# Performance work log

Hardware: AMD Instinct MI355X
Metric: run time of the kernel (lower is better)

## Reference

```python
import jax, jax.numpy as jnp
import numpy as np

NUM_HEADS = 8
KEY_SIZE = 64
VALUE_SIZE = 64
NUM_GROUPS = 3 * NUM_HEADS  # 24
C = NUM_HEADS * (2 * KEY_SIZE + VALUE_SIZE)  # 1536
EPS = 1e-5


def setup_inputs() -> dict:
    key = jax.random.key(0)
    k1, k2, k3 = jax.random.split(key, 3)
    x = jax.random.normal(k1, (8, C, 32, 32), dtype=jnp.float32)
    # GroupNorm affine params (torch default ones/zeros, perturbed for non-trivial grads)
    gn_weight = 1.0 + 0.1 * jax.random.normal(k2, (C,), dtype=jnp.float32)
    gn_bias = 0.1 * jax.random.normal(k3, (C,), dtype=jnp.float32)
    return {"x": x, "gn_weight": gn_weight, "gn_bias": gn_bias}


def _group_norm(x, weight, bias):
    B, Cc, H, W = x.shape
    xg = x.reshape(B, NUM_GROUPS, -1)  # [B, G, (C/G)*H*W]
    mean = jnp.mean(xg, axis=-1, keepdims=True)
    var = jnp.var(xg, axis=-1, keepdims=True)
    xn = ((xg - mean) * jax.lax.rsqrt(var + EPS)).reshape(B, Cc, H, W)
    return xn * weight[:, None, None] + bias[:, None, None]


def reference(x, gn_weight, gn_bias):
    NH, KS, VS = NUM_HEADS, KEY_SIZE, VALUE_SIZE
    B, Cc, H, W = x.shape
    xn = _group_norm(x, gn_weight, gn_bias)
    xr = xn.reshape(B, NH, 2 * KS + VS, H * W)  # [B, NH, 2KS+VS, NK]
    k = xr[:, :, :KS]            # [B, NH, KS, NK]
    q = xr[:, :, KS:2 * KS]      # [B, NH, KS, NK]
    v = xr[:, :, 2 * KS:]        # [B, NH, VS, NK]
    # saliency = q^T @ k / sqrt(KS) -> [B, NH, NKq, NKk]
    sal = jnp.einsum('bhcq,bhck->bhqk', q, k) / jnp.sqrt(jnp.float32(KS))
    mask = jax.nn.softmax(sal, axis=-1)
    # out = v @ mask^T -> [B, NH, VS, NKq]
    out = jnp.einsum('bhvk,bhqk->bhvq', v, mask)
    return out.reshape(B, NH * VS, H, W)
```

## Files before the change

### kernel.cpp

```cpp
#include <hip/hip_runtime.h>
#include <hip/hip_bf16.h>


typedef __attribute__((ext_vector_type(8))) short bf16x8;
typedef __attribute__((ext_vector_type(4))) float f32x4;
typedef __attribute__((ext_vector_type(16))) float f32x16;
typedef unsigned short u16;
typedef unsigned int u32;

#define SM_SCALE 0.18033688f
#define SM_OFF   8.0f

__device__ __forceinline__ u32 pack2(float a, float b) {
    union { float f; u32 u; } ua, ub; ua.f = a; ub.f = b;
    return __builtin_amdgcn_perm(ub.u + 0x8000u, ua.u + 0x8000u, 0x07060302u);
}
union BB { uint4 u; bf16x8 v; };

__device__ __forceinline__ f32x16 zero16() {
    f32x16 z;
#pragma unroll
    for (int i = 0; i < 16; ++i) z[i] = 0.f;
    return z;
}

__device__ __forceinline__ void swap32(u32 a, u32 b, int hi, u32& ret0, u32& ret1) {
#if __has_builtin(__builtin_amdgcn_permlane32_swap)
    (void)hi;
    auto sw = __builtin_amdgcn_permlane32_swap(a, b, false, false);
    ret0 = sw[0]; ret1 = sw[1];
#else
    u32 pa = __shfl_xor(a, 32), pb = __shfl_xor(b, 32);
    ret0 = hi ? pb : a;
    ret1 = hi ? b : pa;
#endif
}

__global__ __launch_bounds__(256) void gn_partial(const float* __restrict__ x,
                                                  float* __restrict__ partials) {
    int blk = blockIdx.x;
    const float4* p = (const float4*)(x + (size_t)blk * 8192);
    int t = threadIdx.x;
    float s1a = 0.f, s2a = 0.f, s1b = 0.f, s2b = 0.f;
#pragma unroll
    for (int i = 0; i < 8; i += 2) {
        float4 va = p[t + i * 256];
        float4 vb = p[t + (i + 1) * 256];
        s1a += va.x + va.y + va.z + va.w;
        s2a += va.x*va.x + va.y*va.y + va.z*va.z + va.w*va.w;
        s1b += vb.x + vb.y + vb.z + vb.w;
        s2b += vb.x*vb.x + vb.y*vb.y + vb.z*vb.z + vb.w*vb.w;
    }
    float s1 = s1a + s1b, s2 = s2a + s2b;
    for (int off = 32; off > 0; off >>= 1) {
        s1 += __shfl_down(s1, off);
        s2 += __shfl_down(s2, off);
    }
    __shared__ float a1[4], a2[4];
    int wave = t >> 6, lane = t & 63;
    if (lane == 0) { a1[wave] = s1; a2[wave] = s2; }
    __syncthreads();
    if (t == 0) {
        partials[blk * 2 + 0] = a1[0] + a1[1] + a1[2] + a1[3];
        partials[blk * 2 + 1] = a2[0] + a2[1] + a2[2] + a2[3];
    }
}

__device__ __forceinline__ void group_stats(const float* __restrict__ partials,
                                            int bg, float& mean, float& rstd) {
    float s1 = 0.f, s2 = 0.f;
#pragma unroll
    for (int j = 0; j < 8; ++j) {
        s1 += partials[(bg * 8 + j) * 2 + 0];
        s2 += partials[(bg * 8 + j) * 2 + 1];
    }
    mean = s1 * (1.f / 65536.f);
    float var = s2 * (1.f / 65536.f) - mean * mean;
    rstd = rsqrtf(var + 1e-5f);
}

__global__ __launch_bounds__(256) void pack_kernel(
    const float* __restrict__ x, const float* __restrict__ gamma,
    const float* __restrict__ beta, const float* __restrict__ partials,
    u16* __restrict__ Qn, u16* __restrict__ Kn, u16* __restrict__ Vn)
{
    const int st = blockIdx.x >> 6, pair = blockIdx.x & 63;
    const int b = pair >> 3, h = pair & 7;
    const float* xb = x + (size_t)b * 1536 * 1024;
    float ms[3], rs[3];
    group_stats(partials, b * 24 + 3 * h + 0, ms[0], rs[0]);
    group_stats(partials, b * 24 + 3 * h + 1, ms[1], rs[1]);
    group_stats(partials, b * 24 + 3 * h + 2, ms[2], rs[2]);

    const int t = threadIdx.x;
    __shared__ u32 Tsh[64][33];

    const int cp = t >> 4;
    const int s4 = (t & 15) * 4;
    const int sgl = st * 64 + s4;

    for (int t2 = 0; t2 < 2; ++t2) {
        if (t2) __syncthreads();
#pragma unroll
        for (int dc = 0; dc < 2; ++dc) {
            int cg0 = h * 192 + t2 * 64 + dc * 32 + cp * 2;
            float4 va = *(const float4*)(xb + (size_t)cg0 * 1024 + sgl);
            float4 vb = *(const float4*)(xb + (size_t)(cg0 + 1) * 1024 + sgl);
            float w0 = gamma[cg0] * rs[t2],     b0 = beta[cg0] - ms[t2] * w0;
            float w1 = gamma[cg0 + 1] * rs[t2], b1 = beta[cg0 + 1] - ms[t2] * w1;
            int col = dc * 16 + cp;
            Tsh[s4 + 0][col] = pack2(va.x * w0 + b0, vb.x * w1 + b1);
            Tsh[s4 + 1][col] = pack2(va.y * w0 + b0, vb.y * w1 + b1);
            Tsh[s4 + 2][col] = pack2(va.z * w0 + b0, vb.z * w1 + b1);
            Tsh[s4 + 3][col] = pack2(va.w * w0 + b0, vb.w * w1 + b1);
        }
        __syncthreads();
        u16* dst = (t2 ? Qn : Kn) + (size_t)pair * 65536 + (size_t)st * 64 * 64;
#pragma unroll
        for (int p = 0; p < 2; ++p) {
            int row = p * 32 + (t >> 3);
            int c8 = (t & 7) * 4;
            uint4 o;
            o.x = Tsh[row][c8 + 0]; o.y = Tsh[row][c8 + 1];
            o.z = Tsh[row][c8 + 2]; o.w = Tsh[row][c8 + 3];
            *(uint4*)(dst + (size_t)row * 64 + c8 * 2) = o;
        }
    }
    {
#pragma unroll
        for (int dc = 0; dc < 4; ++dc) {
            int c = dc * 16 + (t >> 4);
            int cg = h * 192 + 128 + c;
            float4 v = *(const float4*)(xb + (size_t)cg * 1024 + sgl);
            float wsc = gamma[cg] * rs[2];
            float bsc = beta[cg] - ms[2] * wsc;
            uint2 o;
            o.x = pack2(v.x * wsc + bsc, v.y * wsc + bsc);
            o.y = pack2(v.z * wsc + bsc, v.w * wsc + bsc);
            *(uint2*)(Vn + (size_t)pair * 65536 + (size_t)c * 1024 + sgl) = o;
        }
    }
}

__global__ __launch_bounds__(256, 2) void attn_kernel(
    const u16* __restrict__ Qn, const u16* __restrict__ Kn,
    const u16* __restrict__ Vn, float* __restrict__ out)
{
    const int bid = blockIdx.x;
    const int qt = bid >> 6;
    const int pair = bid & 63;
    const int tid = threadIdx.x;
    const int w = tid >> 6;
    const int lane = tid & 63;
    const int li = lane & 31;
    const int hi = lane >> 5;

    __shared__ uint4 KT[2][512];
    __shared__ uint4 VT[2][512];

    const u16* Qp = Qn + (size_t)pair * 65536;
    const u16* Kp = Kn + (size_t)pair * 65536;
    const u16* Vp = Vn + (size_t)pair * 65536;

    const int j0 = tid * 2;
    const int srow = j0 >> 3;
    const int sch  = j0 & 7;
    const int sx   = srow & 7;
    const int idx0 = srow * 8 + (sch ^ sx);
    const int idx1 = srow * 8 + ((sch + 1) ^ sx);

    const int q0 = qt * 128 + w * 32;
    bf16x8 bq[4];
#pragma unroll
    for (int cs = 0; cs < 4; ++cs)
        bq[cs] = *(const bf16x8*)(Qp + (size_t)(q0 + li) * 64 + cs * 16 + hi * 8);

    f32x16 oacc[2];
    oacc[0] = zero16(); oacc[1] = zero16();
    float lsum = 0.f;

    const int x7 = li & 7;

    uint4 s0, s1, s2, s3;
    s0 = *(const uint4*)(Kp + (size_t)j0 * 8);
    s1 = *(const uint4*)(Kp + (size_t)j0 * 8 + 8);
    s2 = *(const uint4*)(Vp + (size_t)srow * 1024 + sch * 8);
    s3 = *(const uint4*)(Vp + (size_t)srow * 1024 + sch * 8 + 8);
    KT[0][idx0] = s0; KT[0][idx1] = s1;
    VT[0][idx0] = s2; VT[0][idx1] = s3;
    __syncthreads();

#pragma unroll 2
    for (int kt = 0; kt < 16; ++kt) {
        const int cur = kt & 1;
        if (kt < 15) {
            s0 = *(const uint4*)(Kp + (size_t)(kt + 1) * 4096 + j0 * 8);
            s1 = *(const uint4*)(Kp + (size_t)(kt + 1) * 4096 + j0 * 8 + 8);
            s2 = *(const uint4*)(Vp + (size_t)srow * 1024 + (kt + 1) * 64 + sch * 8);
            s3 = *(const uint4*)(Vp + (size_t)srow * 1024 + (kt + 1) * 64 + sch * 8 + 8);
        }

        f32x16 sf[2];
#pragma unroll
        for (int kf = 0; kf < 2; ++kf) {
            bf16x8 ak[4];
#pragma unroll
            for (int cs = 0; cs < 4; ++cs)
                ak[cs] = ((const BB*)&KT[cur][(kf * 32 + li) * 8 + ((cs * 2 + hi) ^ x7)])->v;
            f32x16 acc = zero16();
            __builtin_amdgcn_s_setprio(1);
#pragma unroll
            for (int cs = 0; cs < 4; ++cs)
                acc = __builtin_amdgcn_mfma_f32_32x32x16_bf16(ak[cs], bq[cs], acc, 0, 0, 0);
            __builtin_amdgcn_s_setprio(0);
            sf[kf] = acc;
        }

        BB pbv[4];
#pragma unroll
        for (int kf = 0; kf < 2; ++kf)
#pragma unroll
            for (int s = 0; s < 2; ++s) {
                float p0 = exp2f(__builtin_fmaf(sf[kf][8 * s + 0], SM_SCALE, -SM_OFF));
                float p1 = exp2f(__builtin_fmaf(sf[kf][8 * s + 1], SM_SCALE, -SM_OFF));
                float p2 = exp2f(__builtin_fmaf(sf[kf][8 * s + 2], SM_SCALE, -SM_OFF));
                float p3 = exp2f(__builtin_fmaf(sf[kf][8 * s + 3], SM_SCALE, -SM_OFF));
                float p4 = exp2f(__builtin_fmaf(sf[kf][8 * s + 4], SM_SCALE, -SM_OFF));
                float p5 = exp2f(__builtin_fmaf(sf[kf][8 * s + 5], SM_SCALE, -SM_OFF));
                float p6 = exp2f(__builtin_fmaf(sf[kf][8 * s + 6], SM_SCALE, -SM_OFF));
                float p7 = exp2f(__builtin_fmaf(sf[kf][8 * s + 7], SM_SCALE, -SM_OFF));
                lsum += ((p0 + p1) + (p2 + p3)) + ((p4 + p5) + (p6 + p7));
                u32 Pa = pack2(p0, p1), Pb = pack2(p2, p3);
                u32 Pc = pack2(p4, p5), Pd = pack2(p6, p7);
                u32 w0, w1, w2, w3;
                swap32(Pa, Pc, hi, w0, w2);
                swap32(Pb, Pd, hi, w1, w3);
                pbv[kf * 2 + s].u = uint4{w0, w1, w2, w3};
            }

#pragma unroll
        for (int vf = 0; vf < 2; ++vf) {
            bf16x8 av[4];
#pragma unroll
            for (int ks = 0; ks < 4; ++ks)
                av[ks] = ((const BB*)&VT[cur][(vf * 32 + li) * 8 + ((ks * 2 + hi) ^ x7)])->v;
            __builtin_amdgcn_s_setprio(1);
#pragma unroll
            for (int ks = 0; ks < 4; ++ks)
                oacc[vf] = __builtin_amdgcn_mfma_f32_32x32x16_bf16(av[ks], pbv[ks].v, oacc[vf], 0, 0, 0);
            __builtin_amdgcn_s_setprio(0);
        }

        if (kt < 15) {
            const int nxt = cur ^ 1;
            KT[nxt][idx0] = s0; KT[nxt][idx1] = s1;
            VT[nxt][idx0] = s2; VT[nxt][idx1] = s3;
        }
        __syncthreads();
    }

    lsum += __shfl_xor(lsum, 32);
    float invl = 1.f / lsum;
    float* ob = out + (size_t)pair * 65536 + q0 + li;
#pragma unroll
    for (int vf = 0; vf < 2; ++vf)
#pragma unroll
        for (int r = 0; r < 16; ++r) {
            int v = vf * 32 + (r & 3) + 8 * (r >> 2) + 4 * hi;
            ob[(size_t)v * 1024] = oacc[vf][r] * invl;
        }
}

extern "C" void kernel_launch(void* const* d_in, const int* in_sizes, int n_in,
                              void* d_out, int out_size, void* d_ws, size_t ws_size,
                              hipStream_t stream) {
    const float* x     = (const float*)d_in[0];
    const float* gamma = (const float*)d_in[1];
    const float* beta  = (const float*)d_in[2];
    float* out = (float*)d_out;

    float* partials = (float*)d_ws;
    u16* Qn = (u16*)((char*)d_ws + 32768);
    u16* Kn = Qn + (size_t)64 * 65536;
    u16* Vn = Kn + (size_t)64 * 65536;

    gn_partial<<<1536, 256, 0, stream>>>(x, partials);
    pack_kernel<<<1024, 256, 0, stream>>>(x, gamma, beta, partials, Qn, Kn, Vn);
    attn_kernel<<<512, 256, 0, stream>>>(Qn, Kn, Vn, out);
}
```

Baseline: 131.6 us.

## Fuse GroupNorm normalize and bf16 pack into attention kernel, drop pack pass

```diff
diff --git a/kernel.cpp b/kernel.cpp
--- a/kernel.cpp
+++ b/kernel.cpp
@@ -79,101 +79,70 @@
     rstd = rsqrtf(var + 1e-5f);
 }
 
-__global__ __launch_bounds__(256) void pack_kernel(
+__global__ __launch_bounds__(256, 2) void attn_fused(
     const float* __restrict__ x, const float* __restrict__ gamma,
     const float* __restrict__ beta, const float* __restrict__ partials,
-    u16* __restrict__ Qn, u16* __restrict__ Kn, u16* __restrict__ Vn)
-{
-    const int st = blockIdx.x >> 6, pair = blockIdx.x & 63;
-    const int b = pair >> 3, h = pair & 7;
-    const float* xb = x + (size_t)b * 1536 * 1024;
-    float ms[3], rs[3];
-    group_stats(partials, b * 24 + 3 * h + 0, ms[0], rs[0]);
-    group_stats(partials, b * 24 + 3 * h + 1, ms[1], rs[1]);
-    group_stats(partials, b * 24 + 3 * h + 2, ms[2], rs[2]);
-
-    const int t = threadIdx.x;
-    __shared__ u32 Tsh[64][33];
-
-    const int cp = t >> 4;
-    const int s4 = (t & 15) * 4;
-    const int sgl = st * 64 + s4;
-
-    for (int t2 = 0; t2 < 2; ++t2) {
-        if (t2) __syncthreads();
-#pragma unroll
-        for (int dc = 0; dc < 2; ++dc) {
-            int cg0 = h * 192 + t2 * 64 + dc * 32 + cp * 2;
-            float4 va = *(const float4*)(xb + (size_t)cg0 * 1024 + sgl);
-            float4 vb = *(const float4*)(xb + (size_t)(cg0 + 1) * 1024 + sgl);
-            float w0 = gamma[cg0] * rs[t2],     b0 = beta[cg0] - ms[t2] * w0;
-            float w1 = gamma[cg0 + 1] * rs[t2], b1 = beta[cg0 + 1] - ms[t2] * w1;
-            int col = dc * 16 + cp;
-            Tsh[s4 + 0][col] = pack2(va.x * w0 + b0, vb.x * w1 + b1);
-            Tsh[s4 + 1][col] = pack2(va.y * w0 + b0, vb.y * w1 + b1);
-            Tsh[s4 + 2][col] = pack2(va.z * w0 + b0, vb.z * w1 + b1);
-            Tsh[s4 + 3][col] = pack2(va.w * w0 + b0, vb.w * w1 + b1);
-        }
-        __syncthreads();
-        u16* dst = (t2 ? Qn : Kn) + (size_t)pair * 65536 + (size_t)st * 64 * 64;
-#pragma unroll
-        for (int p = 0; p < 2; ++p) {
-            int row = p * 32 + (t >> 3);
-            int c8 = (t & 7) * 4;
-            uint4 o;
-            o.x = Tsh[row][c8 + 0]; o.y = Tsh[row][c8 + 1];
-            o.z = Tsh[row][c8 + 2]; o.w = Tsh[row][c8 + 3];
-            *(uint4*)(dst + (size_t)row * 64 + c8 * 2) = o;
-        }
-    }
-    {
-#pragma unroll
-        for (int dc = 0; dc < 4; ++dc) {
-            int c = dc * 16 + (t >> 4);
-            int cg = h * 192 + 128 + c;
-            float4 v = *(const float4*)(xb + (size_t)cg * 1024 + sgl);
-            float wsc = gamma[cg] * rs[2];
-            float bsc = beta[cg] - ms[2] * wsc;
-            uint2 o;
-            o.x = pack2(v.x * wsc + bsc, v.y * wsc + bsc);
-            o.y = pack2(v.z * wsc + bsc, v.w * wsc + bsc);
-            *(uint2*)(Vn + (size_t)pair * 65536 + (size_t)c * 1024 + sgl) = o;
-        }
-    }
-}
-
-__global__ __launch_bounds__(256, 2) void attn_kernel(
-    const u16* __restrict__ Qn, const u16* __restrict__ Kn,
-    const u16* __restrict__ Vn, float* __restrict__ out)
+    float* __restrict__ out)
 {
     const int bid = blockIdx.x;
     const int qt = bid >> 6;
     const int pair = bid & 63;
+    const int b = pair >> 3, h = pair & 7;
+    const float* xb = x + (size_t)b * 1536 * 1024;
     const int tid = threadIdx.x;
     const int w = tid >> 6;
     const int lane = tid & 63;
     const int li = lane & 31;
     const int hi = lane >> 5;
 
+    float ms[3], rs[3];
+    group_stats(partials, b * 24 + 3 * h + 0, ms[0], rs[0]);
+    group_stats(partials, b * 24 + 3 * h + 1, ms[1], rs[1]);
+    group_stats(partials, b * 24 + 3 * h + 2, ms[2], rs[2]);
+
     __shared__ uint4 KT[2][512];
     __shared__ uint4 VT[2][512];
 
-    const u16* Qp = Qn + (size_t)pair * 65536;
-    const u16* Kp = Kn + (size_t)pair * 65536;
-    const u16* Vp = Vn + (size_t)pair * 65536;
-
-    const int j0 = tid * 2;
-    const int srow = j0 >> 3;
-    const int sch  = j0 & 7;
-    const int sx   = srow & 7;
-    const int idx0 = srow * 8 + (sch ^ sx);
-    const int idx1 = srow * 8 + ((sch + 1) ^ sx);
+    const int sr = tid & 63;
+    const int cc0 = tid >> 6;
+    float kw[16], kb[16];
+#pragma unroll
+    for (int u = 0; u < 16; ++u) {
+        int c = ((u < 8) ? cc0 : (cc0 + 4)) * 8 + (u & 7);
+        int cg = h * 192 + c;
+        kw[u] = gamma[cg] * rs[0];
+        kb[u] = beta[cg] - ms[0] * kw[u];
+    }
+    const int vcg = h * 192 + 128 + sr;
+    const float vw = gamma[vcg] * rs[2];
+    const float vb = beta[vcg] - ms[2] * vw;
+
+    const int kx = sr & 7;
+    const int kidx0 = sr * 8 + (cc0 ^ kx);
+    const int kidx1 = sr * 8 + ((cc0 + 4) ^ kx);
+    const int vidx0 = sr * 8 + ((cc0 * 2) ^ kx);
+    const int vidx1 = sr * 8 + ((cc0 * 2 + 1) ^ kx);
+
+    const float* kbase = xb + (size_t)(h * 192) * 1024 + sr;
+    const float* vbase = xb + (size_t)vcg * 1024 + cc0 * 16;
 
     const int q0 = qt * 128 + w * 32;
     bf16x8 bq[4];
 #pragma unroll
-    for (int cs = 0; cs < 4; ++cs)
-        bq[cs] = *(const bf16x8*)(Qp + (size_t)(q0 + li) * 64 + cs * 16 + hi * 8);
+    for (int cs = 0; cs < 4; ++cs) {
+        u32 qq[4];
+#pragma unroll
+        for (int jp = 0; jp < 4; ++jp) {
+            int cg = h * 192 + 64 + cs * 16 + hi * 8 + jp * 2;
+            float w0 = gamma[cg] * rs[1],     b0 = beta[cg] - ms[1] * w0;
+            float w1 = gamma[cg + 1] * rs[1], b1 = beta[cg + 1] - ms[1] * w1;
+            float a0 = xb[(size_t)cg * 1024 + q0 + li];
+            float a1 = xb[(size_t)(cg + 1) * 1024 + q0 + li];
+            qq[jp] = pack2(__builtin_fmaf(a0, w0, b0), __builtin_fmaf(a1, w1, b1));
+        }
+        BB tb; tb.u = uint4{qq[0], qq[1], qq[2], qq[3]};
+        bq[cs] = tb.v;
+    }
 
     f32x16 oacc[2];
     oacc[0] = zero16(); oacc[1] = zero16();
@@ -181,24 +150,70 @@
 
     const int x7 = li & 7;
 
-    uint4 s0, s1, s2, s3;
-    s0 = *(const uint4*)(Kp + (size_t)j0 * 8);
-    s1 = *(const uint4*)(Kp + (size_t)j0 * 8 + 8);
-    s2 = *(const uint4*)(Vp + (size_t)srow * 1024 + sch * 8);
-    s3 = *(const uint4*)(Vp + (size_t)srow * 1024 + sch * 8 + 8);
-    KT[0][idx0] = s0; KT[0][idx1] = s1;
-    VT[0][idx0] = s2; VT[0][idx1] = s3;
+    float rk[16], rv[16];
+#define LOAD_TILE(KT_)                                                        \
+    {                                                                         \
+        const float* kp = kbase + (KT_) * 64;                                 \
+        _Pragma("unroll")                                                     \
+        for (int u = 0; u < 16; ++u) {                                        \
+            int c = ((u < 8) ? cc0 : (cc0 + 4)) * 8 + (u & 7);                \
+            rk[u] = kp[(size_t)c * 1024];                                     \
+        }                                                                     \
+        const float* vp = vbase + (KT_) * 64;                                 \
+        _Pragma("unroll")                                                     \
+        for (int f = 0; f < 4; ++f) {                                         \
+            float4 vq = *(const float4*)(vp + f * 4);                         \
+            rv[f * 4 + 0] = vq.x; rv[f * 4 + 1] = vq.y;                       \
+            rv[f * 4 + 2] = vq.z; rv[f * 4 + 3] = vq.w;                       \
+        }                                                                     \
+    }
+#define COMMIT_TILE(BUF_)                                                     \
+    {                                                                         \
+        uint4 ka, kc, va, vc;                                                 \
+        ka.x = pack2(__builtin_fmaf(rk[0], kw[0], kb[0]),                     \
+                     __builtin_fmaf(rk[1], kw[1], kb[1]));                    \
+        ka.y = pack2(__builtin_fmaf(rk[2], kw[2], kb[2]),                     \
+                     __builtin_fmaf(rk[3], kw[3], kb[3]));                    \
+        ka.z = pack2(__builtin_fmaf(rk[4], kw[4], kb[4]),                     \
+                     __builtin_fmaf(rk[5], kw[5], kb[5]));                    \
+        ka.w = pack2(__builtin_fmaf(rk[6], kw[6], kb[6]),                     \
+                     __builtin_fmaf(rk[7], kw[7], kb[7]));                    \
+        kc.x = pack2(__builtin_fmaf(rk[8], kw[8], kb[8]),                     \
+                     __builtin_fmaf(rk[9], kw[9], kb[9]));                    \
+        kc.y = pack2(__builtin_fmaf(rk[10], kw[10], kb[10]),                  \
+                     __builtin_fmaf(rk[11], kw[11], kb[11]));                 \
+        kc.z = pack2(__builtin_fmaf(rk[12], kw[12], kb[12]),                  \
+                     __builtin_fmaf(rk[13], kw[13], kb[13]));                 \
+        kc.w = pack2(__builtin_fmaf(rk[14], kw[14], kb[14]),                  \
+                     __builtin_fmaf(rk[15], kw[15], kb[15]));                 \
+        va.x = pack2(__builtin_fmaf(rv[0], vw, vb),                           \
+                     __builtin_fmaf(rv[1], vw, vb));                          \
+        va.y = pack2(__builtin_fmaf(rv[2], vw, vb),                           \
+                     __builtin_fmaf(rv[3], vw, vb));                          \
+        va.z = pack2(__builtin_fmaf(rv[4], vw, vb),                           \
+                     __builtin_fmaf(rv[5], vw, vb));                          \
+        va.w = pack2(__builtin_fmaf(rv[6], vw, vb),                           \
+                     __builtin_fmaf(rv[7], vw, vb));                          \
+        vc.x = pack2(__builtin_fmaf(rv[8], vw, vb),                           \
+                     __builtin_fmaf(rv[9], vw, vb));                          \
+        vc.y = pack2(__builtin_fmaf(rv[10], vw, vb),                          \
+                     __builtin_fmaf(rv[11], vw, vb));                         \
+        vc.z = pack2(__builtin_fmaf(rv[12], vw, vb),                          \
+                     __builtin_fmaf(rv[13], vw, vb));                         \
+        vc.w = pack2(__builtin_fmaf(rv[14], vw, vb),                          \
+                     __builtin_fmaf(rv[15], vw, vb));                         \
+        KT[BUF_][kidx0] = ka; KT[BUF_][kidx1] = kc;                           \
+        VT[BUF_][vidx0] = va; VT[BUF_][vidx1] = vc;                           \
+    }
+
+    LOAD_TILE(0);
+    COMMIT_TILE(0);
     __syncthreads();
 
 #pragma unroll 2
     for (int kt = 0; kt < 16; ++kt) {
         const int cur = kt & 1;
-        if (kt < 15) {
-            s0 = *(const uint4*)(Kp + (size_t)(kt + 1) * 4096 + j0 * 8);
-            s1 = *(const uint4*)(Kp + (size_t)(kt + 1) * 4096 + j0 * 8 + 8);
-            s2 = *(const uint4*)(Vp + (size_t)srow * 1024 + (kt + 1) * 64 + sch * 8);
-            s3 = *(const uint4*)(Vp + (size_t)srow * 1024 + (kt + 1) * 64 + sch * 8 + 8);
-        }
+        if (kt < 15) LOAD_TILE(kt + 1);
 
         f32x16 sf[2];
 #pragma unroll
@@ -251,11 +266,7 @@
             __builtin_amdgcn_s_setprio(0);
         }
 
-        if (kt < 15) {
-            const int nxt = cur ^ 1;
-            KT[nxt][idx0] = s0; KT[nxt][idx1] = s1;
-            VT[nxt][idx0] = s2; VT[nxt][idx1] = s3;
-        }
+        if (kt < 15) COMMIT_TILE(cur ^ 1);
         __syncthreads();
     }
 
@@ -280,11 +291,7 @@
     float* out = (float*)d_out;
 
     float* partials = (float*)d_ws;
-    u16* Qn = (u16*)((char*)d_ws + 32768);
-    u16* Kn = Qn + (size_t)64 * 65536;
-    u16* Vn = Kn + (size_t)64 * 65536;
 
     gn_partial<<<1536, 256, 0, stream>>>(x, partials);
-    pack_kernel<<<1024, 256, 0, stream>>>(x, gamma, beta, partials, Qn, Kn, Vn);
-    attn_kernel<<<512, 256, 0, stream>>>(Qn, Kn, Vn, out);
-}
+    attn_fused<<<512, 256, 0, stream>>>(x, gamma, beta, partials, out);
+}
```

Measured after the change: 129.6 us. About the same (-1.5%).
